# Performance work log

Measured on AMD Instinct MI355X. Metric: run time of the kernel, lower is better.

The kernel has to match this reference:

```python
import jax, jax.numpy as jnp
import numpy as np

N = 50000
E = 800000
IN_CH = 128
HID = 32
HEADS = 4
OUT_CH = 32
NEG_SLOPE = 0.2


def setup_inputs() -> dict:
    key = jax.random.key(0)
    ks = jax.random.split(key, 12)
    x = jax.random.normal(ks[0], (N, IN_CH), dtype=jnp.float32)
    edge_index = jax.random.randint(ks[1], (2, E), 0, N, dtype=jnp.int64)
    s1 = 1.0 / np.sqrt(IN_CH)
    s2 = 1.0 / np.sqrt(HEADS * HID)
    W1 = jax.random.normal(ks[2], (IN_CH, HEADS * HID), dtype=jnp.float32) * s1
    att_src1 = jax.random.normal(ks[3], (HEADS, HID), dtype=jnp.float32) * s2
    att_dst1 = jax.random.normal(ks[4], (HEADS, HID), dtype=jnp.float32) * s2
    b1 = jnp.zeros((HEADS * HID,), dtype=jnp.float32)
    W2 = jax.random.normal(ks[5], (HEADS * HID, OUT_CH), dtype=jnp.float32) * s2
    att_src2 = jax.random.normal(ks[6], (1, OUT_CH), dtype=jnp.float32) * (1.0 / np.sqrt(OUT_CH))
    att_dst2 = jax.random.normal(ks[7], (1, OUT_CH), dtype=jnp.float32) * (1.0 / np.sqrt(OUT_CH))
    b2 = jnp.zeros((OUT_CH,), dtype=jnp.float32)
    return {"x": x, "edge_index": edge_index, "W1": W1, "att_src1": att_src1,
            "att_dst1": att_dst1, "b1": b1, "W2": W2, "att_src2": att_src2,
            "att_dst2": att_dst2, "b2": b2}


def _gat_layer(x, src, dst, W, att_src, att_dst, bias, heads, out_ch, concat):
    n = x.shape[0]
    xw = (x @ W).reshape(n, heads, out_ch)            # [N,H,C]
    a_src = jnp.einsum('nhc,hc->nh', xw, att_src)     # [N,H]
    a_dst = jnp.einsum('nhc,hc->nh', xw, att_dst)
    e = a_src[src] + a_dst[dst]                        # [E,H]
    e = jnp.where(e > 0, e, NEG_SLOPE * e)             # LeakyReLU(0.2)
    # edge-softmax grouped by destination node (stable)
    e_max = jax.ops.segment_max(e, dst, num_segments=n)
    e_max = jnp.where(jnp.isfinite(e_max), e_max, 0.0)
    e_exp = jnp.exp(e - e_max[dst])
    denom = jax.ops.segment_sum(e_exp, dst, num_segments=n)
    alpha = e_exp / (denom[dst] + 1e-16)               # [E,H]
    msg = xw[src] * alpha[:, :, None]                  # [E,H,C]
    out = jax.ops.segment_sum(msg, dst, num_segments=n)  # [N,H,C]
    if concat:
        out = out.reshape(n, heads * out_ch)
    else:
        out = out.mean(axis=1)
    return out + bias


def reference(x, edge_index, W1, att_src1, att_dst1, b1, W2, att_src2, att_dst2, b2):
    # PyG GATConv adds self-loops by default
    loops = jnp.arange(N, dtype=edge_index.dtype)
    src = jnp.concatenate([edge_index[0], loops])
    dst = jnp.concatenate([edge_index[1], loops])
    h = _gat_layer(x, src, dst, W1, att_src1, att_dst1, b1, HEADS, HID, True)
    h = jax.nn.elu(h)
    # dropout p=0.5 is identity at inference (training=False)
    out = _gat_layer(h, src, dst, W2, att_src2, att_dst2, b2, 1, OUT_CH, False)
    return out
```

## Files before the change

kernel.cpp:

```cpp
#include <hip/hip_runtime.h>
#include <hip/hip_fp16.h>

#define N_NODES 50000
#define E_EDGES 800000
#define ETOT (E_EDGES + N_NODES)
#define IN_CH 128
#define HH 128
#define HEADS 4
#define HID 32
#define OUT_CH 32
#define NEG 0.2f

#define GEMM_BLOCKS ((N_NODES + 127) / 128)
#define FILL_BLOCKS ((ETOT + 1023) / 1024)
#define XP 132

__global__ __launch_bounds__(256, 2) void gemm1_fused(const float* __restrict__ x,
                                                      const float* __restrict__ W1,
                                                      const float* __restrict__ att_s,
                                                      const float* __restrict__ att_d,
                                                      const int* __restrict__ ei,
                                                      __half* __restrict__ xwh,
                                                      float* __restrict__ a1s,
                                                      float* __restrict__ a1d,
                                                      int* __restrict__ deg,
                                                      int* __restrict__ idx) {
    __shared__ float Xs[32][XP];
    __shared__ float Ws[32][XP];
    int t = threadIdx.x;

    if (blockIdx.x >= GEMM_BLOCKS) {
        int base = (blockIdx.x - GEMM_BLOCKS) * 1024 + t;
#pragma unroll
        for (int q = 0; q < 4; ++q) {
            int e = base + q * 256;
            if (e < ETOT) {
                int d = (e < E_EDGES) ? ei[E_EDGES + e] : e - E_EDGES;
                idx[e] = atomicAdd(deg + d, 1);
            }
        }
        return;
    }

    int tx = t & 15, ty = t >> 4;
    int row0 = blockIdx.x * 128;
    float acc[8][8] = {};

    for (int k0 = 0; k0 < IN_CH; k0 += 32) {
#pragma unroll
        for (int p = 0; p < 4; ++p) {
            int i2 = t + p * 256;
            int kk = i2 >> 5, c4 = i2 & 31;
            float4 v = *(const float4*)&W1[(size_t)(k0 + kk) * HH + c4 * 4];
            *(float4*)&Ws[kk][c4 * 4] = v;
        }
#pragma unroll
        for (int p = 0; p < 4; ++p) {
            int i2 = t + p * 256;
            int rr = i2 >> 3, c4 = i2 & 7;
            int row = row0 + rr;
            float4 v = make_float4(0.f, 0.f, 0.f, 0.f);
            if (row < N_NODES) v = *(const float4*)&x[(size_t)row * IN_CH + k0 + c4 * 4];
            Xs[c4 * 4 + 0][rr] = v.x;
            Xs[c4 * 4 + 1][rr] = v.y;
            Xs[c4 * 4 + 2][rr] = v.z;
            Xs[c4 * 4 + 3][rr] = v.w;
        }
        __syncthreads();
#pragma unroll 8
        for (int kk = 0; kk < 32; ++kk) {
            float4 xa0 = *(const float4*)&Xs[kk][ty * 4];
            float4 xa1 = *(const float4*)&Xs[kk][ty * 4 + 64];
            float4 wb0 = *(const float4*)&Ws[kk][tx * 4];
            float4 wb1 = *(const float4*)&Ws[kk][tx * 4 + 64];
            float xa[8] = {xa0.x, xa0.y, xa0.z, xa0.w, xa1.x, xa1.y, xa1.z, xa1.w};
            float wb[8] = {wb0.x, wb0.y, wb0.z, wb0.w, wb1.x, wb1.y, wb1.z, wb1.w};
#pragma unroll
            for (int i = 0; i < 8; ++i)
#pragma unroll
                for (int j = 0; j < 8; ++j)
                    acc[i][j] = fmaf(xa[i], wb[j], acc[i][j]);
        }
        __syncthreads();
    }

    float asr[8], adr[8];
#pragma unroll
    for (int j = 0; j < 8; ++j) {
        int col = tx * 4 + (j & 3) + ((j >> 2) << 6);
        asr[j] = att_s[col];
        adr[j] = att_d[col];
    }
    int hA = tx >> 3;

#pragma unroll
    for (int i = 0; i < 8; ++i) {
        int row = row0 + ty * 4 + (i < 4 ? i : 60 + i);
        if (row < N_NODES) {
            union { __half2 h2; unsigned u; } c0, c1, c2, c3;
            c0.h2 = __floats2half2_rn(acc[i][0], acc[i][1]);
            c1.h2 = __floats2half2_rn(acc[i][2], acc[i][3]);
            c2.h2 = __floats2half2_rn(acc[i][4], acc[i][5]);
            c3.h2 = __floats2half2_rn(acc[i][6], acc[i][7]);
            *(uint2*)&xwh[(size_t)row * HH + tx * 4]      = make_uint2(c0.u, c1.u);
            *(uint2*)&xwh[(size_t)row * HH + tx * 4 + 64] = make_uint2(c2.u, c3.u);
        }
        float psA = 0.f, pdA = 0.f, psB = 0.f, pdB = 0.f;
#pragma unroll
        for (int j = 0; j < 4; ++j) {
            psA = fmaf(acc[i][j], asr[j], psA);
            pdA = fmaf(acc[i][j], adr[j], pdA);
            psB = fmaf(acc[i][j + 4], asr[j + 4], psB);
            pdB = fmaf(acc[i][j + 4], adr[j + 4], pdB);
        }
#pragma unroll
        for (int off = 1; off < 8; off <<= 1) {
            psA += __shfl_xor(psA, off, 16);
            pdA += __shfl_xor(pdA, off, 16);
            psB += __shfl_xor(psB, off, 16);
            pdB += __shfl_xor(pdB, off, 16);
        }
        if ((tx & 7) == 0 && row < N_NODES) {
            a1s[row * 4 + hA]     = psA;
            a1d[row * 4 + hA]     = pdA;
            a1s[row * 4 + hA + 2] = psB;
            a1d[row * 4 + hA + 2] = pdB;
        }
    }
}

__device__ __forceinline__ int block_incl_scan(int v, int t) {
    for (int off = 1; off < 64; off <<= 1) {
        int n = __shfl_up(v, off, 64);
        if ((t & 63) >= off) v += n;
    }
    __shared__ int wsum[4];
    if ((t & 63) == 63) wsum[t >> 6] = v;
    __syncthreads();
    int w = t >> 6;
    if (w > 0) {
        int add = 0;
        for (int k = 0; k < w; ++k) add += wsum[k];
        v += add;
    }
    __syncthreads();
    return v;
}

#define NCHUNK ((N_NODES + 255) / 256)

__global__ void scan_s1(const int* __restrict__ deg, int* __restrict__ rowptr,
                        int* __restrict__ partials) {
    int t = threadIdx.x;
    int i = blockIdx.x * 256 + t;
    int v = (i < N_NODES) ? deg[i] : 0;
    int s = block_incl_scan(v, t);
    if (i < N_NODES) rowptr[i + 1] = s;
    if (t == 255) partials[blockIdx.x] = s;
}

__global__ void scan_s2(int* __restrict__ partials) {
    int t = threadIdx.x;
    int v = (t < NCHUNK) ? partials[t] : 0;
    int s = block_incl_scan(v, t);
    if (t < NCHUNK) partials[t] = s;
}

__global__ void scan_s3(int* __restrict__ rowptr, const int* __restrict__ partials) {
    int i = blockIdx.x * blockDim.x + threadIdx.x;
    if (i == 0) rowptr[0] = 0;
    if (i < N_NODES) {
        int c = i >> 8;
        if (c > 0) rowptr[i + 1] += partials[c - 1];
    }
}

__global__ void place_csr(const int* __restrict__ ei, const int* __restrict__ idx,
                          const int* __restrict__ rowptr, int* __restrict__ csr_src) {
    int e = blockIdx.x * blockDim.x + threadIdx.x;
    if (e >= ETOT) return;
    int s, d;
    if (e < E_EDGES) { s = ei[e]; d = ei[E_EDGES + e]; }
    else { s = e - E_EDGES; d = s; }
    csr_src[rowptr[d] + idx[e]] = s;
}

__global__ void gather1_g2(const int* __restrict__ rowptr, const int* __restrict__ csr_src,
                           const float* __restrict__ a1s, const float* __restrict__ a1d,
                           const __half* __restrict__ xwh,
                           const float* __restrict__ b1, const float* __restrict__ W2,
                           const float* __restrict__ att_s2, const float* __restrict__ att_d2,
                           __half* __restrict__ hw2h,
                           float* __restrict__ a2s, float* __restrict__ a2d) {
    __shared__ float Wl[HH * OUT_CH];
    __shared__ float hs[8][HH];
    int t = threadIdx.x;
    for (int i = t; i < HH * OUT_CH; i += 256) Wl[i] = W2[i];
    __syncthreads();

    int wid = t >> 5;
    int d = blockIdx.x * 8 + wid;
    int l = t & 31;
    int h = l >> 3;
    float ad = a1d[d * 4 + h];
    int p0 = rowptr[d], p1 = rowptr[d + 1];
    float acc0 = 0.f, acc1 = 0.f, acc2 = 0.f, acc3 = 0.f, wsum = 0.f;
    union { float2 f2; __half2 h2[2]; } u0, u1, u2, u3;
    int p = p0;
    for (; p + 3 < p1; p += 4) {
        int s0 = csr_src[p], s1 = csr_src[p + 1], s2 = csr_src[p + 2], s3 = csr_src[p + 3];
        float v0 = a1s[s0 * 4 + h] + ad; v0 = v0 > 0.f ? v0 : NEG * v0;
        float v1 = a1s[s1 * 4 + h] + ad; v1 = v1 > 0.f ? v1 : NEG * v1;
        float v2 = a1s[s2 * 4 + h] + ad; v2 = v2 > 0.f ? v2 : NEG * v2;
        float v3 = a1s[s3 * 4 + h] + ad; v3 = v3 > 0.f ? v3 : NEG * v3;
        float w0 = __expf(v0), w1 = __expf(v1), w2 = __expf(v2), w3 = __expf(v3);
        u0.f2 = *(const float2*)&xwh[(size_t)s0 * HH + 4 * l];
        u1.f2 = *(const float2*)&xwh[(size_t)s1 * HH + 4 * l];
        u2.f2 = *(const float2*)&xwh[(size_t)s2 * HH + 4 * l];
        u3.f2 = *(const float2*)&xwh[(size_t)s3 * HH + 4 * l];
#define FM(k, W) { float2 fa = __half22float2(u##k.h2[0]); float2 fb = __half22float2(u##k.h2[1]); \
                   acc0 = fmaf(W, fa.x, acc0); acc1 = fmaf(W, fa.y, acc1); \
                   acc2 = fmaf(W, fb.x, acc2); acc3 = fmaf(W, fb.y, acc3); }
        FM(0, w0) FM(1, w1) FM(2, w2) FM(3, w3)
#undef FM
        wsum += (w0 + w1) + (w2 + w3);
    }
    for (; p < p1; ++p) {
        int s = csr_src[p];
        float v = a1s[s * 4 + h] + ad; v = v > 0.f ? v : NEG * v;
        float w = __expf(v);
        u0.f2 = *(const float2*)&xwh[(size_t)s * HH + 4 * l];
        float2 fa = __half22float2(u0.h2[0]);
        float2 fb = __half22float2(u0.h2[1]);
        acc0 = fmaf(w, fa.x, acc0); acc1 = fmaf(w, fa.y, acc1);
        acc2 = fmaf(w, fb.x, acc2); acc3 = fmaf(w, fb.y, acc3);
        wsum += w;
    }
    float r = 1.f / (wsum + 1e-16f);
    float4 bv = *(const float4*)&b1[4 * l];
    float h0 = acc0 * r + bv.x;
    float h1 = acc1 * r + bv.y;
    float h2v = acc2 * r + bv.z;
    float h3v = acc3 * r + bv.w;
    h0  = h0  > 0.f ? h0  : (__expf(h0)  - 1.f);
    h1  = h1  > 0.f ? h1  : (__expf(h1)  - 1.f);
    h2v = h2v > 0.f ? h2v : (__expf(h2v) - 1.f);
    h3v = h3v > 0.f ? h3v : (__expf(h3v) - 1.f);
    *(float4*)&hs[wid][4 * l] = make_float4(h0, h1, h2v, h3v);

    const float* hrow = hs[wid];
    const float* wcol = &Wl[l];
    float acc = 0.f;
#pragma unroll 8
    for (int j = 0; j < 128; ++j) acc = fmaf(hrow[j], wcol[j * OUT_CH], acc);

    hw2h[(size_t)d * OUT_CH + l] = __float2half_rn(acc);

    float ps = acc * att_s2[l], pd = acc * att_d2[l];
#pragma unroll
    for (int off = 16; off; off >>= 1) {
        ps += __shfl_xor(ps, off, 32);
        pd += __shfl_xor(pd, off, 32);
    }
    if (l == 0) { a2s[d] = ps; a2d[d] = pd; }
}

__global__ void gather2(const int* __restrict__ rowptr, const int* __restrict__ csr_src,
                        const float* __restrict__ a2s, const float* __restrict__ a2d,
                        const __half* __restrict__ hw2h, const float* __restrict__ b2,
                        float* __restrict__ out) {
    int t = threadIdx.x;
    int d = blockIdx.x * 8 + (t >> 5);
    if (d >= N_NODES) return;
    int o = t & 31;
    float ad = a2d[d];
    int p0 = rowptr[d], p1 = rowptr[d + 1];
    float acc = 0.f, wsum = 0.f;
    int p = p0;
    for (; p + 3 < p1; p += 4) {
        int s0 = csr_src[p], s1 = csr_src[p + 1], s2 = csr_src[p + 2], s3 = csr_src[p + 3];
        float v0 = a2s[s0] + ad; v0 = v0 > 0.f ? v0 : NEG * v0;
        float v1 = a2s[s1] + ad; v1 = v1 > 0.f ? v1 : NEG * v1;
        float v2 = a2s[s2] + ad; v2 = v2 > 0.f ? v2 : NEG * v2;
        float v3 = a2s[s3] + ad; v3 = v3 > 0.f ? v3 : NEG * v3;
        float w0 = __expf(v0), w1 = __expf(v1), w2 = __expf(v2), w3 = __expf(v3);
        float x0 = __half2float(hw2h[(size_t)s0 * OUT_CH + o]);
        float x1 = __half2float(hw2h[(size_t)s1 * OUT_CH + o]);
        float x2 = __half2float(hw2h[(size_t)s2 * OUT_CH + o]);
        float x3 = __half2float(hw2h[(size_t)s3 * OUT_CH + o]);
        acc = fmaf(w0, x0, acc); acc = fmaf(w1, x1, acc);
        acc = fmaf(w2, x2, acc); acc = fmaf(w3, x3, acc);
        wsum += (w0 + w1) + (w2 + w3);
    }
    for (; p < p1; ++p) {
        int s = csr_src[p];
        float v = a2s[s] + ad; v = v > 0.f ? v : NEG * v;
        float w = __expf(v);
        acc = fmaf(w, __half2float(hw2h[(size_t)s * OUT_CH + o]), acc);
        wsum += w;
    }
    out[(size_t)d * OUT_CH + o] = acc / (wsum + 1e-16f) + b2[o];
}

extern "C" void kernel_launch(void* const* d_in, const int* in_sizes, int n_in,
                              void* d_out, int out_size, void* d_ws, size_t ws_size,
                              hipStream_t stream) {
    const float* x   = (const float*)d_in[0];
    const int*   ei  = (const int*)d_in[1];
    const float* W1  = (const float*)d_in[2];
    const float* as1 = (const float*)d_in[3];
    const float* ad1 = (const float*)d_in[4];
    const float* b1  = (const float*)d_in[5];
    const float* W2  = (const float*)d_in[6];
    const float* as2 = (const float*)d_in[7];
    const float* ad2 = (const float*)d_in[8];
    const float* b2  = (const float*)d_in[9];
    float* out = (float*)d_out;
    float* ws  = (float*)d_ws;

    __half* xwh   = (__half*)ws;
    __half* hw2h  = (__half*)(ws + 3200000);
    float* a1s    = ws + 4000000;
    float* a1d    = ws + 4200000;
    float* a2s    = ws + 4400000;
    float* a2d    = ws + 4450000;
    int*   deg    = (int*)(ws + 4500000);
    int*   rowptr = (int*)(ws + 4550000);
    int*   parts  = (int*)(ws + 4600016);
    int*   csr_src= (int*)(ws + 4600272);
    int*   idx    = (int*)(ws + 5450272);

    hipMemsetAsync(deg, 0, (size_t)N_NODES * sizeof(int), stream);

    gemm1_fused<<<GEMM_BLOCKS + FILL_BLOCKS, 256, 0, stream>>>(
        x, W1, as1, ad1, ei, xwh, a1s, a1d, deg, idx);

    scan_s1  <<<NCHUNK, 256, 0, stream>>>(deg, rowptr, parts);
    scan_s2  <<<1, 256, 0, stream>>>(parts);
    scan_s3  <<<(N_NODES + 255) / 256, 256, 0, stream>>>(rowptr, parts);
    place_csr<<<(ETOT + 255) / 256, 256, 0, stream>>>(ei, idx, rowptr, csr_src);

    gather1_g2<<<N_NODES / 8, 256, 0, stream>>>(rowptr, csr_src, a1s, a1d, xwh,
                                                b1, W2, as2, ad2, hw2h, a2s, a2d);

    gather2  <<<(N_NODES + 7) / 8, 256, 0, stream>>>(rowptr, csr_src, a2s, a2d, hw2h, b2, out);
}
```

Before: 156.5 us.

## Replace global atomic degree counting with per-block shared-memory histograms

The CSR degree count now uses 16 blocks, each building shared-memory histograms over a quarter of the node range at a time, instead of global atomics spread across many blocks. Per-block counts are combined by a new column-scan kernel into degrees and per-block offsets, and place_csr adds the block offset to each edge's local index. This removes global atomic contention and the memset, but leaves only 16 blocks to scan all edges four times, so the histogram phase may become the critical path next to the GEMM.

```diff
diff --git a/kernel.cpp b/kernel.cpp
--- a/kernel.cpp
+++ b/kernel.cpp
@@ -12,7 +12,10 @@
 #define NEG 0.2f
 
 #define GEMM_BLOCKS ((N_NODES + 127) / 128)
-#define FILL_BLOCKS ((ETOT + 1023) / 1024)
+#define NB_HIST 16
+#define EPB (ETOT / NB_HIST)
+#define QN 12544
+#define CNT_STRIDE 50176
 #define XP 132
 
 __global__ __launch_bounds__(256, 2) void gemm1_fused(const float* __restrict__ x,
@@ -23,25 +26,41 @@
                                                       __half* __restrict__ xwh,
                                                       float* __restrict__ a1s,
                                                       float* __restrict__ a1d,
-                                                      int* __restrict__ deg,
-                                                      int* __restrict__ idx) {
-    __shared__ float Xs[32][XP];
-    __shared__ float Ws[32][XP];
+                                                      int* __restrict__ idx,
+                                                      int* __restrict__ cnt) {
+    __shared__ __align__(16) char smem[QN * 4];
     int t = threadIdx.x;
 
     if (blockIdx.x >= GEMM_BLOCKS) {
-        int base = (blockIdx.x - GEMM_BLOCKS) * 1024 + t;
-#pragma unroll
+        int b = blockIdx.x - GEMM_BLOCKS;
+        int* hist = (int*)smem;
+        const int e0 = b * EPB, e1 = e0 + EPB;
         for (int q = 0; q < 4; ++q) {
-            int e = base + q * 256;
-            if (e < ETOT) {
-                int d = (e < E_EDGES) ? ei[E_EDGES + e] : e - E_EDGES;
-                idx[e] = atomicAdd(deg + d, 1);
+            int dlo = q * QN;
+            int dcnt = (N_NODES - dlo < QN) ? (N_NODES - dlo) : QN;
+            for (int i = t; i < QN; i += 256) hist[i] = 0;
+            __syncthreads();
+            for (int i0 = e0 + t; i0 < e1; i0 += 1024) {
+#pragma unroll
+                for (int k = 0; k < 4; ++k) {
+                    int e = i0 + k * 256;
+                    if (e < e1) {
+                        int d = (e < E_EDGES) ? ei[E_EDGES + e] : e - E_EDGES;
+                        int r = d - dlo;
+                        if ((unsigned)r < (unsigned)dcnt)
+                            idx[e] = atomicAdd(&hist[r], 1);
+                    }
+                }
             }
+            __syncthreads();
+            for (int i = t; i < dcnt; i += 256) cnt[b * CNT_STRIDE + dlo + i] = hist[i];
+            __syncthreads();
         }
         return;
     }
 
+    float* Xs = (float*)smem;
+    float* Ws = (float*)(smem + 32 * XP * 4);
     int tx = t & 15, ty = t >> 4;
     int row0 = blockIdx.x * 128;
     float acc[8][8] = {};
@@ -52,7 +71,7 @@
             int i2 = t + p * 256;
             int kk = i2 >> 5, c4 = i2 & 31;
             float4 v = *(const float4*)&W1[(size_t)(k0 + kk) * HH + c4 * 4];
-            *(float4*)&Ws[kk][c4 * 4] = v;
+            *(float4*)&Ws[kk * XP + c4 * 4] = v;
         }
 #pragma unroll
         for (int p = 0; p < 4; ++p) {
@@ -61,18 +80,18 @@
             int row = row0 + rr;
             float4 v = make_float4(0.f, 0.f, 0.f, 0.f);
             if (row < N_NODES) v = *(const float4*)&x[(size_t)row * IN_CH + k0 + c4 * 4];
-            Xs[c4 * 4 + 0][rr] = v.x;
-            Xs[c4 * 4 + 1][rr] = v.y;
-            Xs[c4 * 4 + 2][rr] = v.z;
-            Xs[c4 * 4 + 3][rr] = v.w;
+            Xs[(c4 * 4 + 0) * XP + rr] = v.x;
+            Xs[(c4 * 4 + 1) * XP + rr] = v.y;
+            Xs[(c4 * 4 + 2) * XP + rr] = v.z;
+            Xs[(c4 * 4 + 3) * XP + rr] = v.w;
         }
         __syncthreads();
 #pragma unroll 8
         for (int kk = 0; kk < 32; ++kk) {
-            float4 xa0 = *(const float4*)&Xs[kk][ty * 4];
-            float4 xa1 = *(const float4*)&Xs[kk][ty * 4 + 64];
-            float4 wb0 = *(const float4*)&Ws[kk][tx * 4];
-            float4 wb1 = *(const float4*)&Ws[kk][tx * 4 + 64];
+            float4 xa0 = *(const float4*)&Xs[kk * XP + ty * 4];
+            float4 xa1 = *(const float4*)&Xs[kk * XP + ty * 4 + 64];
+            float4 wb0 = *(const float4*)&Ws[kk * XP + tx * 4];
+            float4 wb1 = *(const float4*)&Ws[kk * XP + tx * 4 + 64];
             float xa[8] = {xa0.x, xa0.y, xa0.z, xa0.w, xa1.x, xa1.y, xa1.z, xa1.w};
             float wb[8] = {wb0.x, wb0.y, wb0.z, wb0.w, wb1.x, wb1.y, wb1.z, wb1.w};
 #pragma unroll
@@ -129,6 +148,19 @@
     }
 }
 
+__global__ void col_scan(int* __restrict__ cnt, int* __restrict__ deg) {
+    int d = blockIdx.x * 256 + threadIdx.x;
+    if (d >= N_NODES) return;
+    int s = 0;
+#pragma unroll
+    for (int b = 0; b < NB_HIST; ++b) {
+        int c = cnt[b * CNT_STRIDE + d];
+        cnt[b * CNT_STRIDE + d] = s;
+        s += c;
+    }
+    deg[d] = s;
+}
+
 __device__ __forceinline__ int block_incl_scan(int v, int t) {
     for (int off = 1; off < 64; off <<= 1) {
         int n = __shfl_up(v, off, 64);
@@ -176,13 +208,15 @@
 }
 
 __global__ void place_csr(const int* __restrict__ ei, const int* __restrict__ idx,
-                          const int* __restrict__ rowptr, int* __restrict__ csr_src) {
+                          const int* __restrict__ rowptr, const int* __restrict__ cnt,
+                          int* __restrict__ csr_src) {
     int e = blockIdx.x * blockDim.x + threadIdx.x;
     if (e >= ETOT) return;
     int s, d;
     if (e < E_EDGES) { s = ei[e]; d = ei[E_EDGES + e]; }
     else { s = e - E_EDGES; d = s; }
-    csr_src[rowptr[d] + idx[e]] = s;
+    int b = e / EPB;
+    csr_src[rowptr[d] + cnt[b * CNT_STRIDE + d] + idx[e]] = s;
 }
 
 __global__ void gather1_g2(const int* __restrict__ rowptr, const int* __restrict__ csr_src,
@@ -329,16 +363,16 @@
     int*   parts  = (int*)(ws + 4600016);
     int*   csr_src= (int*)(ws + 4600272);
     int*   idx    = (int*)(ws + 5450272);
-
-    hipMemsetAsync(deg, 0, (size_t)N_NODES * sizeof(int), stream);
-
-    gemm1_fused<<<GEMM_BLOCKS + FILL_BLOCKS, 256, 0, stream>>>(
-        x, W1, as1, ad1, ei, xwh, a1s, a1d, deg, idx);
-
+    int*   cnt    = (int*)(ws + 6300272);
+
+    gemm1_fused<<<GEMM_BLOCKS + NB_HIST, 256, 0, stream>>>(
+        x, W1, as1, ad1, ei, xwh, a1s, a1d, idx, cnt);
+
+    col_scan <<<(N_NODES + 255) / 256, 256, 0, stream>>>(cnt, deg);
     scan_s1  <<<NCHUNK, 256, 0, stream>>>(deg, rowptr, parts);
     scan_s2  <<<1, 256, 0, stream>>>(parts);
     scan_s3  <<<(N_NODES + 255) / 256, 256, 0, stream>>>(rowptr, parts);
-    place_csr<<<(ETOT + 255) / 256, 256, 0, stream>>>(ei, idx, rowptr, csr_src);
+    place_csr<<<(ETOT + 255) / 256, 256, 0, stream>>>(ei, idx, rowptr, cnt, csr_src);
 
     gather1_g2<<<N_NODES / 8, 256, 0, stream>>>(rowptr, csr_src, a1s, a1d, xwh,
                                                 b1, W2, as2, ad2, hw2h, a2s, a2d);
```

Result: slower. 311.1 us (+98.8%).
